# Performance work log

Measured on AMD Instinct MI355X. Metric: run time of the kernel, lower is better.

Reference implementation:

```python
import jax, jax.numpy as jnp
import numpy as np

A = 9          # angRes
MIND = -4      # mindisp
MAXD = 4       # maxdisp
C0 = A // 2
BDR = C0 * MAXD  # per-view zero padding


def setup_inputs() -> dict:
    key = jax.random.key(0)
    k1, k2, k3 = jax.random.split(key, 3)
    b, c, h, w = 1, 32, 192, 192
    cout = 128
    x = jax.random.normal(k1, (b, c, A * A, h, w), dtype=jnp.float32)
    mask = jax.random.uniform(k2, (b, A * A, h, w), dtype=jnp.float32)
    W = jax.random.normal(k3, (cout, A * A), dtype=jnp.float32) / np.sqrt(A * A)
    return {"x": x, "mask": mask, "W": W}


def reference(x, mask, W):
    # x: [b, c, A*A, h, w], mask: [b, A*A, h, w], W: [cout, A*A] (grouped 1x1 conv, groups=c)
    b, c, aa, h, w = x.shape
    m = W.shape[0] // c  # outputs per group
    Wr = W.reshape(c, m, A, A)
    # per-view layout [b, a1, a2, c, h, w], zero-pad spatially by BDR (equivalent to mosaic padding)
    xv = x.reshape(b, c, A, A, h, w).transpose(0, 2, 3, 1, 4, 5)
    xp = jnp.pad(xv, ((0, 0), (0, 0), (0, 0), (0, 0), (BDR, BDR), (BDR, BDR)))
    maskv = mask.reshape(b, A, A, h, w)
    mask_avg = jnp.mean(mask, axis=1)  # [b, h, w]
    ar = jnp.arange(A)
    outs = []
    for d in range(MIND, MAXD + 1):
        # tap (p,q) of the dilated AxA unfold reads padded view (p,q) shifted by start_p/start_q
        starts = C0 * (d - MIND) - ar * d                      # [A]
        ridx = starts[:, None] + jnp.arange(h)[None, :]        # [A, h]
        cidx = starts[:, None] + jnp.arange(w)[None, :]        # [A, w]
        t = jnp.take_along_axis(xp, ridx[None, :, None, None, :, None], axis=4)
        t = jnp.take_along_axis(t, cidx[None, None, :, None, None, :], axis=5)  # [b,A,A,c,h,w]
        # fuse mask modulation + grouped 1x1 conv over the A*A taps
        o = jnp.einsum('bpqchw,bpqhw,cmpq->bcmhw', t, maskv, Wr)
        outs.append(o.reshape(b, c * m, h, w) / mask_avg[:, None, :, :])
    return jnp.stack(outs, axis=2)  # [b, cout, n_disp, h, w]
```

## Files before the change

kernel.cpp:

```cpp
#include <hip/hip_runtime.h>


#define AA   81
#define HH   192
#define WW   192
#define HW   (HH * WW)
#define NC   32
#define MM   4
#define ND   9

#define RG      48
#define RITEMS  (RG * RG / 4)

__global__ __launch_bounds__(256)
void buildcost_kernel(const float* __restrict__ x,
                      const float* __restrict__ mask,
                      const float* __restrict__ Wt,
                      float* __restrict__ out) {
    __shared__ float  wlds[AA * MM];
    __shared__ float4 buf[2][RITEMS];

    const int lin  = blockIdx.x;
    const int xcd  = lin & 7;
    const int slot = lin >> 3;
    const int cgrp = slot / 144;
    const int sp   = slot - cgrp * 144;
    const int c    = xcd + (cgrp << 3);
    const int by   = sp / 12;
    const int bx   = sp - by * 12;

    const int tid = threadIdx.x;
    const int tx  = tid & 15;
    const int ty  = tid >> 4;
    const int j   = bx * 16 + tx;
    const int i   = by * 16 + ty;
    const int pix = i * WW + j;

    for (int idx = tid; idx < AA * MM; idx += 256) {
        const int t = idx >> 2;
        const int m = idx & 3;
        wlds[idx] = Wt[(c * MM + m) * AA + t];
    }

    const int y0 = by * 16 - 16;
    const int x0 = bx * 16 - 16;

    int off0, off1, off2;
    bool v0, v1, v2;
    {
        const int i0 = tid,        r0 = i0 / 12, c0 = (i0 - r0 * 12) * 4;
        const int i1 = tid + 256,  r1 = i1 / 12, c1 = (i1 - r1 * 12) * 4;
        const int i2 = tid + 512,  r2 = i2 / 12, c2 = (i2 - r2 * 12) * 4;
        const int gy0 = y0 + r0, gx0 = x0 + c0;
        const int gy1 = y0 + r1, gx1 = x0 + c1;
        const int gy2 = y0 + r2, gx2 = x0 + c2;
        v0 = ((unsigned)gy0 < (unsigned)HH) & ((unsigned)gx0 < (unsigned)WW);
        v1 = ((unsigned)gy1 < (unsigned)HH) & ((unsigned)gx1 < (unsigned)WW);
        v2 = (i2 < RITEMS) & ((unsigned)gy2 < (unsigned)HH) & ((unsigned)gx2 < (unsigned)WW);
        off0 = v0 ? (gy0 * WW + gx0) : 0;
        off1 = v1 ? (gy1 * WW + gx1) : 0;
        off2 = v2 ? (gy2 * WW + gx2) : 0;
    }
    const bool interior = (bx >= 1) & (bx <= 10) & (by >= 1) & (by <= 10);

    const float* __restrict__ xc = x + (size_t)c * AA * HW;

    float4 s0, s1, s2;
    const float4 zf4 = {0.f, 0.f, 0.f, 0.f};

#define STAGE_LOAD(XT)                                                  \
    do {                                                                \
        if (interior) {                                                 \
            s0 = *(const float4*)((XT) + off0);                         \
            s1 = *(const float4*)((XT) + off1);                         \
            s2 = zf4;                                                   \
            if (tid < 64) s2 = *(const float4*)((XT) + off2);           \
        } else {                                                        \
            s0 = zf4; s1 = zf4; s2 = zf4;                               \
            if (v0) s0 = *(const float4*)((XT) + off0);                 \
            if (v1) s1 = *(const float4*)((XT) + off1);                 \
            if (v2) s2 = *(const float4*)((XT) + off2);                 \
        }                                                               \
    } while (0)

    float acc[ND][MM];
#pragma unroll
    for (int dd = 0; dd < ND; ++dd)
#pragma unroll
        for (int m = 0; m < MM; ++m) acc[dd][m] = 0.f;

    const float* __restrict__ xt = xc;
    STAGE_LOAD(xt);
    {
        float4* wb = &buf[0][0];
        wb[tid]       = s0;
        wb[tid + 256] = s1;
        if (tid < 64) wb[tid + 512] = s2;
    }
    float mval_next = mask[pix];
    __syncthreads();

    const int lbase = (ty + 16) * RG + (tx + 16);
    float msum = 0.f;
    int p = 0, q = 0;
    int cur = 0;

#pragma unroll 1
    for (int t = 0; t < AA; ++t) {
        const float mval = mval_next;
        const bool  more = (t + 1 < AA);

        if (more) {
            xt += HW;
            STAGE_LOAD(xt);
            mval_next = mask[(size_t)(t + 1) * HW + pix];
        }

        msum += mval;
        const float4 w4 = *(const float4*)&wlds[t * 4];
        const int kp = 4 - p;
        const int kq = 4 - q;
        const int lstep = kp * RG + kq;
        const float* lb = (const float*)&buf[cur][0];

#pragma unroll
        for (int dd = 0; dd < ND; ++dd) {
            const float v = lb[lbase + (dd - 4) * lstep];
            const float s = v * mval;
            acc[dd][0] += s * w4.x;
            acc[dd][1] += s * w4.y;
            acc[dd][2] += s * w4.z;
            acc[dd][3] += s * w4.w;
        }

        if (more) {
            float4* wb = &buf[cur ^ 1][0];
            wb[tid]       = s0;
            wb[tid + 256] = s1;
            if (tid < 64) wb[tid + 512] = s2;
        }
        __syncthreads();
        cur ^= 1;
        if (++q == 9) { q = 0; ++p; }
    }

    const float inv = (float)AA / msum;

#pragma unroll
    for (int m = 0; m < MM; ++m)
#pragma unroll
        for (int dd = 0; dd < ND; ++dd)
            out[((size_t)(c * MM + m) * ND + dd) * HW + pix] = acc[dd][m] * inv;
}

extern "C" void kernel_launch(void* const* d_in, const int* in_sizes, int n_in,
                              void* d_out, int out_size, void* d_ws, size_t ws_size,
                              hipStream_t stream) {
    const float* x    = (const float*)d_in[0];
    const float* mask = (const float*)d_in[1];
    const float* Wt   = (const float*)d_in[2];
    float* out        = (float*)d_out;

    dim3 grid(12 * 12 * NC);
    dim3 block(256);
    buildcost_kernel<<<grid, block, 0, stream>>>(x, mask, Wt, out);
}
```

Before: 770.3 us.

## Stream view tiles into a 4-deep LDS ring via direct global-to-LDS loads

Replaces the register-staged double buffer with a 4-slot LDS ring filled by global_load_lds, keeping three views in flight and waiting with counted vmcnt plus a raw s_barrier per step. Out-of-bounds halo slots are zeroed once up front and skipped afterwards. The mask value is also folded into the four weights, so each tap needs one fewer multiply. This targets global-load latency and removes the VGPR round-trip and LDS store instructions. In exchange it relies on hand-counted vmcnt values and on the wave-uniform __any predicates matching the loads each wave actually issues.

```diff
diff --git a/kernel.cpp b/kernel.cpp
--- a/kernel.cpp
+++ b/kernel.cpp
@@ -11,6 +11,13 @@
 
 #define RG      48
 #define RITEMS  (RG * RG / 4)
+#define RING    4
+
+__device__ __forceinline__ void glds16(const float* g, float4* l) {
+    __builtin_amdgcn_global_load_lds(
+        (const __attribute__((address_space(1))) void*)g,
+        (__attribute__((address_space(3))) void*)l, 16, 0, 0);
+}
 
 __global__ __launch_bounds__(256)
 void buildcost_kernel(const float* __restrict__ x,
@@ -18,7 +25,7 @@
                       const float* __restrict__ Wt,
                       float* __restrict__ out) {
     __shared__ float  wlds[AA * MM];
-    __shared__ float4 buf[2][RITEMS];
+    __shared__ float4 buf[RING][RITEMS];
 
     const int lin  = blockIdx.x;
     const int xcd  = lin & 7;
@@ -29,12 +36,13 @@
     const int by   = sp / 12;
     const int bx   = sp - by * 12;
 
-    const int tid = threadIdx.x;
-    const int tx  = tid & 15;
-    const int ty  = tid >> 4;
-    const int j   = bx * 16 + tx;
-    const int i   = by * 16 + ty;
-    const int pix = i * WW + j;
+    const int tid  = threadIdx.x;
+    const int wave = tid >> 6;
+    const int tx   = tid & 15;
+    const int ty   = tid >> 4;
+    const int j    = bx * 16 + tx;
+    const int i    = by * 16 + ty;
+    const int pix  = i * WW + j;
 
     for (int idx = tid; idx < AA * MM; idx += 256) {
         const int t = idx >> 2;
@@ -56,32 +64,47 @@
         const int gy2 = y0 + r2, gx2 = x0 + c2;
         v0 = ((unsigned)gy0 < (unsigned)HH) & ((unsigned)gx0 < (unsigned)WW);
         v1 = ((unsigned)gy1 < (unsigned)HH) & ((unsigned)gx1 < (unsigned)WW);
-        v2 = (i2 < RITEMS) & ((unsigned)gy2 < (unsigned)HH) & ((unsigned)gx2 < (unsigned)WW);
-        off0 = v0 ? (gy0 * WW + gx0) : 0;
-        off1 = v1 ? (gy1 * WW + gx1) : 0;
-        off2 = v2 ? (gy2 * WW + gx2) : 0;
+        v2 = ((unsigned)gy2 < (unsigned)HH) & ((unsigned)gx2 < (unsigned)WW);
+        off0 = gy0 * WW + gx0;
+        off1 = gy1 * WW + gx1;
+        off2 = gy2 * WW + gx2;
     }
     const bool interior = (bx >= 1) & (bx <= 10) & (by >= 1) & (by <= 10);
 
+    if (!interior) {
+        const float4 z = {0.f, 0.f, 0.f, 0.f};
+        if (!v0) { for (int r = 0; r < RING; ++r) buf[r][tid] = z; }
+        if (!v1) { for (int r = 0; r < RING; ++r) buf[r][tid + 256] = z; }
+        if (tid < 64 && !v2) { for (int r = 0; r < RING; ++r) buf[r][tid + 512] = z; }
+    }
+    asm volatile("s_waitcnt lgkmcnt(0)" ::: "memory");
+
+    int gw = 1 + (__any((int)v0) ? 1 : 0) + (__any((int)v1) ? 1 : 0);
+    if (wave == 0) gw += (__any((int)v2) ? 1 : 0);
+    const int W2 = 2 * gw;
+
     const float* __restrict__ xc = x + (size_t)c * AA * HW;
 
-    float4 s0, s1, s2;
-    const float4 zf4 = {0.f, 0.f, 0.f, 0.f};
-
-#define STAGE_LOAD(XT)                                                  \
-    do {                                                                \
-        if (interior) {                                                 \
-            s0 = *(const float4*)((XT) + off0);                         \
-            s1 = *(const float4*)((XT) + off1);                         \
-            s2 = zf4;                                                   \
-            if (tid < 64) s2 = *(const float4*)((XT) + off2);           \
-        } else {                                                        \
-            s0 = zf4; s1 = zf4; s2 = zf4;                               \
-            if (v0) s0 = *(const float4*)((XT) + off0);                 \
-            if (v1) s1 = *(const float4*)((XT) + off1);                 \
-            if (v2) s2 = *(const float4*)((XT) + off2);                 \
-        }                                                               \
-    } while (0)
+    {
+        const float* xt = xc;
+#pragma unroll
+        for (int tt = 0; tt < 3; ++tt) {
+            float4* dst = &buf[tt][0];
+            if (interior) {
+                glds16(xt + off0, dst + (wave << 6));
+                glds16(xt + off1, dst + 256 + (wave << 6));
+                if (wave == 0) glds16(xt + off2, dst + 512);
+            } else {
+                if (v0) glds16(xt + off0, dst + (wave << 6));
+                if (v1) glds16(xt + off1, dst + 256 + (wave << 6));
+                if (wave == 0) { if (v2) glds16(xt + off2, dst + 512); }
+            }
+            xt += HW;
+        }
+    }
+    float mv0 = mask[pix];
+    float mv1 = mask[HW + pix];
+    float mv2 = mask[2 * HW + pix];
 
     float acc[ND][MM];
 #pragma unroll
@@ -89,58 +112,63 @@
 #pragma unroll
         for (int m = 0; m < MM; ++m) acc[dd][m] = 0.f;
 
-    const float* __restrict__ xt = xc;
-    STAGE_LOAD(xt);
-    {
-        float4* wb = &buf[0][0];
-        wb[tid]       = s0;
-        wb[tid + 256] = s1;
-        if (tid < 64) wb[tid + 512] = s2;
-    }
-    float mval_next = mask[pix];
-    __syncthreads();
-
     const int lbase = (ty + 16) * RG + (tx + 16);
     float msum = 0.f;
     int p = 0, q = 0;
-    int cur = 0;
 
 #pragma unroll 1
     for (int t = 0; t < AA; ++t) {
-        const float mval = mval_next;
-        const bool  more = (t + 1 < AA);
+        if (t == 0) {
+            asm volatile("s_waitcnt vmcnt(0)" ::: "memory");
+        } else if (W2 == 8) {
+            asm volatile("s_waitcnt vmcnt(8)" ::: "memory");
+        } else if (W2 == 6) {
+            asm volatile("s_waitcnt vmcnt(6)" ::: "memory");
+        } else if (W2 == 4) {
+            asm volatile("s_waitcnt vmcnt(4)" ::: "memory");
+        } else {
+            asm volatile("s_waitcnt vmcnt(2)" ::: "memory");
+        }
+        __builtin_amdgcn_s_barrier();
 
-        if (more) {
-            xt += HW;
-            STAGE_LOAD(xt);
-            mval_next = mask[(size_t)(t + 1) * HW + pix];
-        }
+        const float mval = mv0;
+        mv0 = mv1; mv1 = mv2;
+        msum += mval;
 
-        msum += mval;
         const float4 w4 = *(const float4*)&wlds[t * 4];
+        const float wx = w4.x * mval;
+        const float wy = w4.y * mval;
+        const float wz = w4.z * mval;
+        const float ww = w4.w * mval;
+
         const int kp = 4 - p;
         const int kq = 4 - q;
         const int lstep = kp * RG + kq;
-        const float* lb = (const float*)&buf[cur][0];
+        const float* lb = (const float*)&buf[t & (RING - 1)][0];
 
 #pragma unroll
         for (int dd = 0; dd < ND; ++dd) {
             const float v = lb[lbase + (dd - 4) * lstep];
-            const float s = v * mval;
-            acc[dd][0] += s * w4.x;
-            acc[dd][1] += s * w4.y;
-            acc[dd][2] += s * w4.z;
-            acc[dd][3] += s * w4.w;
+            acc[dd][0] += v * wx;
+            acc[dd][1] += v * wy;
+            acc[dd][2] += v * wz;
+            acc[dd][3] += v * ww;
         }
 
-        if (more) {
-            float4* wb = &buf[cur ^ 1][0];
-            wb[tid]       = s0;
-            wb[tid + 256] = s1;
-            if (tid < 64) wb[tid + 512] = s2;
+        const int tn = (t + 3 > 80) ? 80 : (t + 3);
+        const float* xt3 = xc + (size_t)tn * HW;
+        float4* dst = &buf[(t + 3) & (RING - 1)][0];
+        if (interior) {
+            glds16(xt3 + off0, dst + (wave << 6));
+            glds16(xt3 + off1, dst + 256 + (wave << 6));
+            if (wave == 0) glds16(xt3 + off2, dst + 512);
+        } else {
+            if (v0) glds16(xt3 + off0, dst + (wave << 6));
+            if (v1) glds16(xt3 + off1, dst + 256 + (wave << 6));
+            if (wave == 0) { if (v2) glds16(xt3 + off2, dst + 512); }
         }
-        __syncthreads();
-        cur ^= 1;
+        mv2 = mask[(size_t)tn * HW + pix];
+
         if (++q == 9) { q = 0; ++p; }
     }
 
```

Result: slower. 798.4 us (+3.6%).
